# Performance work log

Measured on AMD Instinct MI355X. Metric: run time of the kernel, lower is better.

## Reference

```python
import jax, jax.numpy as jnp
import numpy as np

EDGE_DIM = 64
NODE_DIM = 128
N_EDGES = 1_600_000
N_NODES = 50_000
LN_EPS = 1e-5


def setup_inputs() -> dict:
    key = jax.random.key(0)
    k1, k2, k3, k4 = jax.random.split(key, 4)
    edge_attr = jax.random.normal(k1, (N_EDGES, EDGE_DIM), dtype=jnp.float32)
    edge_index = jax.random.randint(k2, (2, N_EDGES), 0, N_NODES, dtype=jnp.int64)
    # Linear(edge_feat_dim, node_feat_dim) params (Kaiming-uniform-ish init)
    bound = 1.0 / np.sqrt(EDGE_DIM)
    W = jax.random.uniform(k3, (EDGE_DIM, NODE_DIM), dtype=jnp.float32, minval=-bound, maxval=bound)
    b = jax.random.uniform(k4, (NODE_DIM,), dtype=jnp.float32, minval=-bound, maxval=bound)
    gamma = jnp.ones((NODE_DIM,), dtype=jnp.float32)
    beta = jnp.zeros((NODE_DIM,), dtype=jnp.float32)
    return {"edge_attr": edge_attr, "W": W, "b": b, "gamma": gamma, "beta": beta,
            "edge_index": edge_index, "num_nodes": N_NODES}


def reference(edge_attr, W, b, gamma, beta, edge_index, num_nodes):
    # Edge transform: Linear -> ReLU -> LayerNorm
    h = jax.nn.relu(edge_attr @ W + b)  # [E, node_dim]
    mu = jnp.mean(h, axis=-1, keepdims=True)
    var = jnp.mean((h - mu) ** 2, axis=-1, keepdims=True)
    h = (h - mu) * jax.lax.rsqrt(var + LN_EPS) * gamma + beta
    src, dst = edge_index[0], edge_index[1]
    # Dual-endpoint scatter-add of transformed edge features
    node_features = (jax.ops.segment_sum(h, dst, num_segments=num_nodes)
                     + jax.ops.segment_sum(h, src, num_segments=num_nodes))  # [N, node_dim]
    ones = jnp.ones(src.shape[0], dtype=h.dtype)
    degree = (jax.ops.segment_sum(ones, src, num_segments=num_nodes)
              + jax.ops.segment_sum(ones, dst, num_segments=num_nodes))  # [N]
    degree = jnp.clip(degree, 1.0)[:, None]
    return node_features / degree
```

## Files before the change

kernel.cpp:

```cpp
#include <hip/hip_runtime.h>

constexpr int ED = 64;
constexpr int ND = 128;

__global__ __launch_bounds__(256, 2)
void edge_scatter_kernel(const float* __restrict__ x,
                         const float* __restrict__ W,
                         const float* __restrict__ bias,
                         const float* __restrict__ gamma,
                         const float* __restrict__ beta,
                         const int*   __restrict__ ei,
                         int E,
                         float* __restrict__ out,
                         float* __restrict__ deg)
{
    const int lane = threadIdx.x & 63;
    const int wid  = (blockIdx.x * (blockDim.x >> 6)) + (threadIdx.x >> 6);
    const int nw   = gridDim.x * (blockDim.x >> 6);

    float w0[ED], w1[ED];
#pragma unroll
    for (int k = 0; k < ED; ++k) {
        w0[k] = W[k * ND + lane];
        w1[k] = W[k * ND + lane + 64];
    }
    const float b0 = bias[lane],  b1 = bias[lane + 64];
    const float g0 = gamma[lane], g1 = gamma[lane + 64];
    const float p0 = beta[lane],  p1 = beta[lane + 64];

    for (int e = wid; e < E; e += nw) {
        const float xv = x[(size_t)e * ED + lane];
        const int   xi = __float_as_int(xv);

        float h0 = b0, h1 = b1;
#pragma unroll
        for (int k = 0; k < ED; ++k) {
            const float xk = __int_as_float(__builtin_amdgcn_readlane(xi, k));
            h0 = fmaf(xk, w0[k], h0);
            h1 = fmaf(xk, w1[k], h1);
        }
        h0 = fmaxf(h0, 0.0f);
        h1 = fmaxf(h1, 0.0f);

        float s  = h0 + h1;
        float s2 = fmaf(h0, h0, h1 * h1);
#pragma unroll
        for (int m = 1; m < 64; m <<= 1) {
            s  += __shfl_xor(s,  m, 64);
            s2 += __shfl_xor(s2, m, 64);
        }
        const float mu  = s * (1.0f / ND);
        const float var = s2 * (1.0f / ND) - mu * mu;
        const float rs  = rsqrtf(var + 1e-5f);
        const float y0  = (h0 - mu) * rs * g0 + p0;
        const float y1  = (h1 - mu) * rs * g1 + p1;

        const int sn = ei[e];
        const int dn = ei[E + e];

        unsafeAtomicAdd(&out[(size_t)dn * ND + lane],      y0);
        unsafeAtomicAdd(&out[(size_t)dn * ND + lane + 64], y1);
        unsafeAtomicAdd(&out[(size_t)sn * ND + lane],      y0);
        unsafeAtomicAdd(&out[(size_t)sn * ND + lane + 64], y1);

        if (lane == 0) unsafeAtomicAdd(&deg[dn], 1.0f);
        if (lane == 1) unsafeAtomicAdd(&deg[sn], 1.0f);
    }
}

__global__ void finalize_kernel(float* __restrict__ out,
                                const float* __restrict__ deg,
                                int total)
{
    const int i = blockIdx.x * blockDim.x + threadIdx.x;
    if (i < total) {
        const float d = fmaxf(deg[i >> 7], 1.0f);
        out[i] = out[i] / d;
    }
}

extern "C" void kernel_launch(void* const* d_in, const int* in_sizes, int n_in,
                              void* d_out, int out_size, void* d_ws, size_t ws_size,
                              hipStream_t stream)
{
    const float* x     = (const float*)d_in[0];
    const float* W     = (const float*)d_in[1];
    const float* bias  = (const float*)d_in[2];
    const float* gamma = (const float*)d_in[3];
    const float* beta  = (const float*)d_in[4];
    const int*   ei    = (const int*)d_in[5];

    const int E       = in_sizes[0] / ED;
    const int n_nodes = out_size / ND;

    float* out = (float*)d_out;
    float* deg = (float*)d_ws;

    hipMemsetAsync(d_out, 0, (size_t)out_size * sizeof(float), stream);
    hipMemsetAsync(d_ws,  0, (size_t)n_nodes * sizeof(float), stream);

    edge_scatter_kernel<<<4096, 256, 0, stream>>>(x, W, bias, gamma, beta,
                                                  ei, E, out, deg);

    finalize_kernel<<<(out_size + 255) / 256, 256, 0, stream>>>(out, deg, out_size);
}
```

Baseline: 1.932 ms.

## Batch four edges per wave and stream packed W from cache instead of registers

Weights are no longer held in 128 per-thread registers. A prep kernel packs each column pair into a float2, and the main loop loads W per k from cache, so launch bounds rise to four blocks per CU. Each wave now processes four edges per iteration, which reuses each W load across four rows and batches the LayerNorm reductions and atomics. The finalize pass is vectorised with float4. The trade is more load traffic from cache per FMA in exchange for higher occupancy and more instruction-level parallelism.

New measurement: 5.145 ms. 166% more time.

```diff
diff --git a/kernel.cpp b/kernel.cpp
--- a/kernel.cpp
+++ b/kernel.cpp
@@ -3,9 +3,18 @@
 constexpr int ED = 64;
 constexpr int ND = 128;
 
-__global__ __launch_bounds__(256, 2)
+__global__ void prep_w_kernel(const float* __restrict__ W, float2* __restrict__ Wp)
+{
+    const int t = blockIdx.x * blockDim.x + threadIdx.x;
+    if (t < ED * 64) {
+        const int k = t >> 6, j = t & 63;
+        Wp[t] = make_float2(W[k * ND + j], W[k * ND + 64 + j]);
+    }
+}
+
+__global__ __launch_bounds__(256, 4)
 void edge_scatter_kernel(const float* __restrict__ x,
-                         const float* __restrict__ W,
+                         const float2* __restrict__ Wp,
                          const float* __restrict__ bias,
                          const float* __restrict__ gamma,
                          const float* __restrict__ beta,
@@ -15,67 +24,134 @@
                          float* __restrict__ deg)
 {
     const int lane = threadIdx.x & 63;
-    const int wid  = (blockIdx.x * (blockDim.x >> 6)) + (threadIdx.x >> 6);
+    const int wid  = blockIdx.x * (blockDim.x >> 6) + (threadIdx.x >> 6);
     const int nw   = gridDim.x * (blockDim.x >> 6);
 
-    float w0[ED], w1[ED];
-#pragma unroll
-    for (int k = 0; k < ED; ++k) {
-        w0[k] = W[k * ND + lane];
-        w1[k] = W[k * ND + lane + 64];
-    }
     const float b0 = bias[lane],  b1 = bias[lane + 64];
     const float g0 = gamma[lane], g1 = gamma[lane + 64];
     const float p0 = beta[lane],  p1 = beta[lane + 64];
 
-    for (int e = wid; e < E; e += nw) {
-        const float xv = x[(size_t)e * ED + lane];
-        const int   xi = __float_as_int(xv);
+    const int ngroups = E >> 2;
 
+    for (int g = wid; g < ngroups; g += nw) {
+        const int e0 = g << 2;
+
+        const int xi0 = __float_as_int(x[(size_t)(e0 + 0) * ED + lane]);
+        const int xi1 = __float_as_int(x[(size_t)(e0 + 1) * ED + lane]);
+        const int xi2 = __float_as_int(x[(size_t)(e0 + 2) * ED + lane]);
+        const int xi3 = __float_as_int(x[(size_t)(e0 + 3) * ED + lane]);
+
+        float h00 = b0, h01 = b1, h10 = b0, h11 = b1;
+        float h20 = b0, h21 = b1, h30 = b0, h31 = b1;
+#pragma unroll
+        for (int k = 0; k < ED; ++k) {
+            const float2 w = Wp[k * 64 + lane];
+            const float x0 = __int_as_float(__builtin_amdgcn_readlane(xi0, k));
+            const float x1 = __int_as_float(__builtin_amdgcn_readlane(xi1, k));
+            const float x2 = __int_as_float(__builtin_amdgcn_readlane(xi2, k));
+            const float x3 = __int_as_float(__builtin_amdgcn_readlane(xi3, k));
+            h00 = fmaf(x0, w.x, h00); h01 = fmaf(x0, w.y, h01);
+            h10 = fmaf(x1, w.x, h10); h11 = fmaf(x1, w.y, h11);
+            h20 = fmaf(x2, w.x, h20); h21 = fmaf(x2, w.y, h21);
+            h30 = fmaf(x3, w.x, h30); h31 = fmaf(x3, w.y, h31);
+        }
+        h00 = fmaxf(h00, 0.f); h01 = fmaxf(h01, 0.f);
+        h10 = fmaxf(h10, 0.f); h11 = fmaxf(h11, 0.f);
+        h20 = fmaxf(h20, 0.f); h21 = fmaxf(h21, 0.f);
+        h30 = fmaxf(h30, 0.f); h31 = fmaxf(h31, 0.f);
+
+        float s0 = h00 + h01, q0 = fmaf(h00, h00, h01 * h01);
+        float s1 = h10 + h11, q1 = fmaf(h10, h10, h11 * h11);
+        float s2 = h20 + h21, q2 = fmaf(h20, h20, h21 * h21);
+        float s3 = h30 + h31, q3 = fmaf(h30, h30, h31 * h31);
+#pragma unroll
+        for (int m = 1; m < 64; m <<= 1) {
+            s0 += __shfl_xor(s0, m, 64); q0 += __shfl_xor(q0, m, 64);
+            s1 += __shfl_xor(s1, m, 64); q1 += __shfl_xor(q1, m, 64);
+            s2 += __shfl_xor(s2, m, 64); q2 += __shfl_xor(q2, m, 64);
+            s3 += __shfl_xor(s3, m, 64); q3 += __shfl_xor(q3, m, 64);
+        }
+        const float inv = 1.0f / ND;
+        const float mu0 = s0 * inv, rs0 = rsqrtf(q0 * inv - mu0 * mu0 + 1e-5f);
+        const float mu1 = s1 * inv, rs1 = rsqrtf(q1 * inv - mu1 * mu1 + 1e-5f);
+        const float mu2 = s2 * inv, rs2 = rsqrtf(q2 * inv - mu2 * mu2 + 1e-5f);
+        const float mu3 = s3 * inv, rs3 = rsqrtf(q3 * inv - mu3 * mu3 + 1e-5f);
+
+        const float y00 = (h00 - mu0) * rs0 * g0 + p0, y01 = (h01 - mu0) * rs0 * g1 + p1;
+        const float y10 = (h10 - mu1) * rs1 * g0 + p0, y11 = (h11 - mu1) * rs1 * g1 + p1;
+        const float y20 = (h20 - mu2) * rs2 * g0 + p0, y21 = (h21 - mu2) * rs2 * g1 + p1;
+        const float y30 = (h30 - mu3) * rs3 * g0 + p0, y31 = (h31 - mu3) * rs3 * g1 + p1;
+
+        const int sn0 = ei[e0 + 0], dn0 = ei[E + e0 + 0];
+        const int sn1 = ei[e0 + 1], dn1 = ei[E + e0 + 1];
+        const int sn2 = ei[e0 + 2], dn2 = ei[E + e0 + 2];
+        const int sn3 = ei[e0 + 3], dn3 = ei[E + e0 + 3];
+
+        unsafeAtomicAdd(&out[(size_t)dn0 * ND + lane],      y00);
+        unsafeAtomicAdd(&out[(size_t)dn0 * ND + 64 + lane], y01);
+        unsafeAtomicAdd(&out[(size_t)sn0 * ND + lane],      y00);
+        unsafeAtomicAdd(&out[(size_t)sn0 * ND + 64 + lane], y01);
+        unsafeAtomicAdd(&out[(size_t)dn1 * ND + lane],      y10);
+        unsafeAtomicAdd(&out[(size_t)dn1 * ND + 64 + lane], y11);
+        unsafeAtomicAdd(&out[(size_t)sn1 * ND + lane],      y10);
+        unsafeAtomicAdd(&out[(size_t)sn1 * ND + 64 + lane], y11);
+        unsafeAtomicAdd(&out[(size_t)dn2 * ND + lane],      y20);
+        unsafeAtomicAdd(&out[(size_t)dn2 * ND + 64 + lane], y21);
+        unsafeAtomicAdd(&out[(size_t)sn2 * ND + lane],      y20);
+        unsafeAtomicAdd(&out[(size_t)sn2 * ND + 64 + lane], y21);
+        unsafeAtomicAdd(&out[(size_t)dn3 * ND + lane],      y30);
+        unsafeAtomicAdd(&out[(size_t)dn3 * ND + 64 + lane], y31);
+        unsafeAtomicAdd(&out[(size_t)sn3 * ND + lane],      y30);
+        unsafeAtomicAdd(&out[(size_t)sn3 * ND + 64 + lane], y31);
+
+        int nid = dn0;
+        if (lane == 1) nid = dn1;
+        if (lane == 2) nid = dn2;
+        if (lane == 3) nid = dn3;
+        if (lane == 4) nid = sn0;
+        if (lane == 5) nid = sn1;
+        if (lane == 6) nid = sn2;
+        if (lane == 7) nid = sn3;
+        if (lane < 8) unsafeAtomicAdd(&deg[nid], 1.0f);
+    }
+
+    for (int e = (ngroups << 2) + wid; e < E; e += nw) {
+        const int xi = __float_as_int(x[(size_t)e * ED + lane]);
         float h0 = b0, h1 = b1;
 #pragma unroll
         for (int k = 0; k < ED; ++k) {
+            const float2 w = Wp[k * 64 + lane];
             const float xk = __int_as_float(__builtin_amdgcn_readlane(xi, k));
-            h0 = fmaf(xk, w0[k], h0);
-            h1 = fmaf(xk, w1[k], h1);
+            h0 = fmaf(xk, w.x, h0); h1 = fmaf(xk, w.y, h1);
         }
-        h0 = fmaxf(h0, 0.0f);
-        h1 = fmaxf(h1, 0.0f);
-
-        float s  = h0 + h1;
-        float s2 = fmaf(h0, h0, h1 * h1);
+        h0 = fmaxf(h0, 0.f); h1 = fmaxf(h1, 0.f);
+        float s = h0 + h1, q = fmaf(h0, h0, h1 * h1);
 #pragma unroll
         for (int m = 1; m < 64; m <<= 1) {
-            s  += __shfl_xor(s,  m, 64);
-            s2 += __shfl_xor(s2, m, 64);
+            s += __shfl_xor(s, m, 64); q += __shfl_xor(q, m, 64);
         }
-        const float mu  = s * (1.0f / ND);
-        const float var = s2 * (1.0f / ND) - mu * mu;
-        const float rs  = rsqrtf(var + 1e-5f);
-        const float y0  = (h0 - mu) * rs * g0 + p0;
-        const float y1  = (h1 - mu) * rs * g1 + p1;
-
-        const int sn = ei[e];
-        const int dn = ei[E + e];
-
+        const float mu = s / ND, rs = rsqrtf(q / ND - mu * mu + 1e-5f);
+        const float y0 = (h0 - mu) * rs * g0 + p0, y1 = (h1 - mu) * rs * g1 + p1;
+        const int sn = ei[e], dn = ei[E + e];
         unsafeAtomicAdd(&out[(size_t)dn * ND + lane],      y0);
-        unsafeAtomicAdd(&out[(size_t)dn * ND + lane + 64], y1);
+        unsafeAtomicAdd(&out[(size_t)dn * ND + 64 + lane], y1);
         unsafeAtomicAdd(&out[(size_t)sn * ND + lane],      y0);
-        unsafeAtomicAdd(&out[(size_t)sn * ND + lane + 64], y1);
-
+        unsafeAtomicAdd(&out[(size_t)sn * ND + 64 + lane], y1);
         if (lane == 0) unsafeAtomicAdd(&deg[dn], 1.0f);
         if (lane == 1) unsafeAtomicAdd(&deg[sn], 1.0f);
     }
 }
 
-__global__ void finalize_kernel(float* __restrict__ out,
+__global__ void finalize_kernel(float4* __restrict__ out,
                                 const float* __restrict__ deg,
-                                int total)
+                                int n4)
 {
     const int i = blockIdx.x * blockDim.x + threadIdx.x;
-    if (i < total) {
-        const float d = fmaxf(deg[i >> 7], 1.0f);
-        out[i] = out[i] / d;
+    if (i < n4) {
+        const float d = fmaxf(deg[i >> 5], 1.0f);
+        float4 v = out[i];
+        v.x /= d; v.y /= d; v.z /= d; v.w /= d;
+        out[i] = v;
     }
 }
 
@@ -93,14 +169,18 @@
     const int E       = in_sizes[0] / ED;
     const int n_nodes = out_size / ND;
 
-    float* out = (float*)d_out;
-    float* deg = (float*)d_ws;
+    float*  out = (float*)d_out;
+    float*  deg = (float*)d_ws;
+    float2* Wp  = (float2*)((char*)d_ws + (size_t)n_nodes * sizeof(float));
 
     hipMemsetAsync(d_out, 0, (size_t)out_size * sizeof(float), stream);
     hipMemsetAsync(d_ws,  0, (size_t)n_nodes * sizeof(float), stream);
 
-    edge_scatter_kernel<<<4096, 256, 0, stream>>>(x, W, bias, gamma, beta,
+    prep_w_kernel<<<(ED * 64 + 255) / 256, 256, 0, stream>>>(W, Wp);
+
+    edge_scatter_kernel<<<4096, 256, 0, stream>>>(x, Wp, bias, gamma, beta,
                                                   ei, E, out, deg);
 
-    finalize_kernel<<<(out_size + 255) / 256, 256, 0, stream>>>(out, deg, out_size);
+    finalize_kernel<<<(out_size / 4 + 255) / 256, 256, 0, stream>>>(
+        (float4*)out, deg, out_size / 4);
 }
```
